# Performance work log

Hardware: AMD Instinct MI355X
Metric: run time of the kernel (lower is better)

## Reference

```python
import jax, jax.numpy as jnp
import numpy as np


def setup_inputs() -> dict:
    key = jax.random.key(0)
    ks = jax.random.split(key, 5)
    B, C_in, C_out, H, W, k = 16, 64, 64, 256, 256, 16
    scale = 1.0 / (C_in * C_out)
    return {
        "u": jax.random.normal(ks[0], (B, C_in, H, W), dtype=jnp.float32),
        "W_pos_re": scale * jax.random.normal(ks[1], (C_in, C_out, k, k), dtype=jnp.float32),
        "W_pos_im": scale * jax.random.normal(ks[2], (C_in, C_out, k, k), dtype=jnp.float32),
        "W_neg_re": scale * jax.random.normal(ks[3], (C_in, C_out, k, k), dtype=jnp.float32),
        "W_neg_im": scale * jax.random.normal(ks[4], (C_in, C_out, k, k), dtype=jnp.float32),
    }


def reference(u, W_pos_re, W_pos_im, W_neg_re, W_neg_im):
    B, C_in, H, W = u.shape
    C_out = W_pos_re.shape[1]
    k = W_pos_re.shape[2]
    W_half = W // 2 + 1
    k_h = min(k, H // 2)
    k_w = min(k, W_half)

    R_pos = (W_pos_re + 1j * W_pos_im)[:, :, :k_h, :k_w]  # (C_in, C_out, k_h, k_w)
    R_neg = (W_neg_re + 1j * W_neg_im)[:, :, :k_h, :k_w]

    u_hat = jnp.fft.rfft2(u, norm="ortho")  # (B, C_in, H, W_half) complex

    # spectral multiply on retained modes only
    top = jnp.einsum("bchw,cohw->bohw", u_hat[:, :, :k_h, :k_w], R_pos)
    bot = jnp.einsum("bchw,cohw->bohw", u_hat[:, :, H - k_h:, :k_w], R_neg)

    v_hat = jnp.zeros((B, C_out, H, W_half), dtype=u_hat.dtype)
    v_hat = v_hat.at[:, :, :k_h, :k_w].set(top)
    v_hat = v_hat.at[:, :, H - k_h:, :k_w].set(bot)

    return jnp.fft.irfft2(v_hat, s=(H, W), norm="ortho")  # (B, C_out, H, W) real
```

## Files before the change

kernel.cpp:

```cpp
#include <hip/hip_runtime.h>


#define B_    16
#define H_    256
#define W_    256

#define OFF_CT 0
#define OFF_ST 256
#define OFF_RP 512
#define RP_SZ  (4096*512*2)
#define OFF_U  (OFF_RP + RP_SZ)
#define U_SZ   (512*1024*2)
#define OFF_V  (OFF_U + U_SZ)

typedef const __attribute__((address_space(1))) void g_void;
typedef __attribute__((address_space(3))) void l_void;

__device__ __forceinline__ void load_lds16(const float* g, float* l) {
    __builtin_amdgcn_global_load_lds((g_void*)g, (l_void*)l, 16, 0, 0);
}

__global__ void k_twiddle(float* __restrict__ ws) {
    int t = threadIdx.x;
    double a = 2.0 * 3.14159265358979323846 * (double)t / 256.0;
    ws[OFF_CT + t] = (float)cos(a);
    ws[OFF_ST + t] = (float)sin(a);
}

__global__ __launch_bounds__(256) void k_repack(const float* __restrict__ wpr,
                                                const float* __restrict__ wpi,
                                                const float* __restrict__ wnr,
                                                const float* __restrict__ wni,
                                                float* __restrict__ ws) {
    int co = blockIdx.x, t = threadIdx.x;
    int wm = t & 15;
    float norm = (wm == 0 ? 1.f : 2.f) * (1.f / 65536.f);
    size_t src = (size_t)co * 256 + t;
    float2* rp = (float2*)(ws + OFF_RP) + (size_t)co * 512;
    rp[t]       = make_float2(wpr[src] * norm, wpi[src] * norm);
    rp[t + 256] = make_float2(wnr[src] * norm, wni[src] * norm);
}

__global__ __launch_bounds__(256) void k_fwd1(const float* __restrict__ u,
                                              const float* __restrict__ ws,
                                              float* __restrict__ P) {
    __shared__ __align__(16) float ut[32][256];
    __shared__ float ct[256], st[256];
    int t = threadIdx.x;
    int bc = blockIdx.x >> 3, ch = blockIdx.x & 7;
    ct[t] = ws[OFF_CT + t];
    st[t] = ws[OFF_ST + t];
    const float* ub = u + (size_t)bc * 65536 + ch * 8192;
    int lane = t & 63, w = t >> 6;
    #pragma unroll
    for (int k = 0; k < 8; ++k) {
        int row = w * 8 + k;
        load_lds16(ub + row * 256 + lane * 4, &ut[row][0]);
    }
    asm volatile("s_waitcnt vmcnt(0)" ::: "memory");
    __syncthreads();

    int yl = t & 31, h = t >> 5;
    int wm0 = 2 * h, wm1 = wm0 + 1;
    int j0 = 2 * yl;
    float t0r = ct[(wm0 * j0) & 255], t0i = -st[(wm0 * j0) & 255];
    float t1r = ct[(wm1 * j0) & 255], t1i = -st[(wm1 * j0) & 255];
    float r0r = ct[wm0], r0i = -st[wm0];
    float r1r = ct[wm1], r1i = -st[wm1];
    float bs  = (h & 1) ? -1.f : 1.f;
    float dsg = (h & 1) ? 1.f : -1.f;
    float p0r = 0.f, p0i = 0.f, p1r = 0.f, p1i = 0.f;
    const float* row = &ut[yl][0];
    #pragma unroll 8
    for (int s = 0; s < 64; ++s) {
        int j = j0 + s;
        float u0 = row[j], u1 = row[j + 64], u2 = row[j + 128];
        float u3 = row[(j + 192) & 255];
        float a = u0 + u2, b = u1 + u3, c = u0 - u2, d = u1 - u3;
        float g0 = fmaf(bs, b, a);
        float g1r = c, g1i = dsg * d;
        p0r = fmaf(g0, t0r, p0r);
        p0i = fmaf(g0, t0i, p0i);
        p1r = fmaf(g1r, t1r, fmaf(-g1i, t1i, p1r));
        p1i = fmaf(g1r, t1i, fmaf( g1i, t1r, p1i));
        float n0r = t0r * r0r - t0i * r0i, n0i = t0r * r0i + t0i * r0r;
        float n1r = t1r * r1r - t1i * r1i, n1i = t1r * r1i + t1i * r1r;
        t0r = n0r; t0i = n0i; t1r = n1r; t1i = n1i;
    }
    int y = ch * 32 + yl;
    ((float4*)P)[((size_t)bc * 256 + y) * 8 + h] = make_float4(p0r, p0i, p1r, p1i);
}

__global__ __launch_bounds__(256) void k_fwd2(const float* __restrict__ P,
                                              float* __restrict__ ws) {
    __shared__ float Pl[256][36];
    __shared__ float ct[256], st[256];
    int t = threadIdx.x, bc = blockIdx.x;
    ct[t] = ws[OFF_CT + t];
    st[t] = ws[OFF_ST + t];
    const float4* Pg = (const float4*)(P + (size_t)bc * 8192);
    #pragma unroll
    for (int k = 0; k < 8; ++k) {
        int f4 = t + 256 * k;
        int y = f4 >> 3, q = f4 & 7;
        *(float4*)&Pl[y][q * 4] = Pg[f4];
    }
    __syncthreads();

    int wm = t & 15;
    int v  = t >> 4;
    int m1 = ((v & 3) << 2) | (v >> 2);
    float r1r = ct[m1], r1i = -st[m1];
    int m2i = (16 - m1) & 255;
    float r2r = ct[m2i], r2i = st[m2i];
    float t1r = 1.f, t1i = 0.f, t2r = 1.f, t2i = 0.f;
    float U1r = 0.f, U1i = 0.f, U2r = 0.f, U2i = 0.f;
    int md = m1 & 3;
    #pragma unroll 4
    for (int yy = 0; yy < 64; ++yy) {
        float2 P0 = *(float2*)&Pl[yy][2 * wm];
        float2 P1 = *(float2*)&Pl[yy + 64][2 * wm];
        float2 P2 = *(float2*)&Pl[yy + 128][2 * wm];
        float2 P3 = *(float2*)&Pl[yy + 192][2 * wm];
        float ar = P0.x + P2.x, ai = P0.y + P2.y;
        float br = P1.x + P3.x, bi = P1.y + P3.y;
        float cr = P0.x - P2.x, ci = P0.y - P2.y;
        float dr = P1.x - P3.x, di = P1.y - P3.y;
        float gr, gi;
        if (md == 0)      { gr = ar + br; gi = ai + bi; }
        else if (md == 1) { gr = cr + di; gi = ci - dr; }
        else if (md == 2) { gr = ar - br; gi = ai - bi; }
        else              { gr = cr - di; gi = ci + dr; }
        U1r = fmaf(gr, t1r, fmaf(-gi, t1i, U1r));
        U1i = fmaf(gr, t1i, fmaf( gi, t1r, U1i));
        U2r = fmaf(gr, t2r, fmaf(-gi, t2i, U2r));
        U2i = fmaf(gr, t2i, fmaf( gi, t2r, U2i));
        float n1r = t1r * r1r - t1i * r1i, n1i = t1r * r1i + t1i * r1r;
        float n2r = t2r * r2r - t2i * r2i, n2i = t2r * r2i + t2i * r2r;
        t1r = n1r; t1i = n1i; t2r = n2r; t2i = n2i;
    }
    float2* U = (float2*)(ws + OFF_U);
    U[(size_t)(m1 * 16 + wm) * 1024 + bc]        = make_float2(U1r, U1i);
    U[(size_t)((m1 + 16) * 16 + wm) * 1024 + bc] = make_float2(U2r, U2i);
}

__global__ __launch_bounds__(256) void k_cgemm(float* __restrict__ ws) {
    __shared__ float2 Ul[1024];
    int mw = blockIdx.x, t = threadIdx.x;
    const float2* Ug = (const float2*)(ws + OFF_U) + (size_t)mw * 1024;
    #pragma unroll
    for (int k = 0; k < 4; ++k) Ul[t + 256 * k] = Ug[t + 256 * k];
    __syncthreads();
    int o = t & 63, bq = t >> 6;
    const float2* rp = (const float2*)(ws + OFF_RP);
    float ar[4] = {0.f, 0.f, 0.f, 0.f}, ai[4] = {0.f, 0.f, 0.f, 0.f};
    #pragma unroll 4
    for (int c = 0; c < 64; ++c) {
        float2 R = rp[(size_t)(c * 64 + o) * 512 + mw];
        #pragma unroll
        for (int j = 0; j < 4; ++j) {
            float2 Uv = Ul[(bq * 4 + j) * 64 + c];
            ar[j] = fmaf(Uv.x, R.x, fmaf(-Uv.y, R.y, ar[j]));
            ai[j] = fmaf(Uv.x, R.y, fmaf( Uv.y, R.x, ai[j]));
        }
    }
    float2* Vg = (float2*)(ws + OFF_V);
    #pragma unroll
    for (int j = 0; j < 4; ++j)
        Vg[(size_t)((bq * 4 + j) * 64 + o) * 512 + mw] = make_float2(ar[j], ai[j]);
}

__global__ __launch_bounds__(256) void k_inv(const float* __restrict__ ws,
                                             float* __restrict__ out) {
    __shared__ float Vl[16][68];
    __shared__ float Tl[4][16][36];
    __shared__ float ct[256], st[256];
    int t = threadIdx.x;
    int bo = blockIdx.x >> 2, q = blockIdx.x & 3;
    ct[t] = ws[OFF_CT + t];
    st[t] = ws[OFF_ST + t];
    {
        const float2* Vg = (const float2*)(ws + OFF_V) + (size_t)bo * 512;
        float2 v0 = Vg[t];
        float2 v1 = Vg[t + 256];
        int m = t >> 4, wmv = t & 15;
        Vl[wmv][2 * m]            = v0.x;  Vl[wmv][2 * m + 1]            = v0.y;
        Vl[wmv][2 * (m + 16)]     = v1.x;  Vl[wmv][2 * (m + 16) + 1]     = v1.y;
    }
    __syncthreads();

    int wm4 = t & 15, yb = t >> 4;
    int y0 = q * 16 + yb;
    float vr[32], vi[32];
    #pragma unroll
    for (int m = 0; m < 32; ++m) { vr[m] = Vl[wm4][2 * m]; vi[m] = Vl[wm4][2 * m + 1]; }
    float cy = ct[y0], sy = st[y0];
    float T0r=0,T0i=0,T1r=0,T1i=0,T2r=0,T2i=0,T3r=0,T3i=0;
    float tr = 1.f, ti = 0.f;
    #pragma unroll
    for (int m = 0; m < 32; ++m) {
        if (m == 16) {
            int i16 = (4096 - 16 * y0) & 255;
            tr = ct[i16]; ti = st[i16];
        }
        float hr = vr[m] * tr - vi[m] * ti;
        float hi = vr[m] * ti + vi[m] * tr;
        const int md = m & 3;
        T0r += hr; T0i += hi;
        if (md == 0)      { T1r += hr; T1i += hi; T2r += hr; T2i += hi; T3r += hr; T3i += hi; }
        else if (md == 1) { T1r -= hi; T1i += hr; T2r -= hr; T2i -= hi; T3r += hi; T3i -= hr; }
        else if (md == 2) { T1r -= hr; T1i -= hi; T2r += hr; T2i += hi; T3r -= hr; T3i -= hi; }
        else              { T1r += hi; T1i -= hr; T2r -= hr; T2i -= hi; T3r -= hi; T3i += hr; }
        float nr = tr * cy - ti * sy, ni = tr * sy + ti * cy;
        tr = nr; ti = ni;
    }
    Tl[0][yb][wm4] = T0r; Tl[0][yb][16 + wm4] = T0i;
    Tl[1][yb][wm4] = T1r; Tl[1][yb][16 + wm4] = T1i;
    Tl[2][yb][wm4] = T2r; Tl[2][yb][16 + wm4] = T2i;
    Tl[3][yb][wm4] = T3r; Tl[3][yb][16 + wm4] = T3i;
    __syncthreads();

    int l = t & 63, wv = t >> 6;
    float c0[16], s0[16];
    #pragma unroll
    for (int wm = 0; wm < 16; ++wm) {
        int idx = (wm * l) & 255;
        c0[wm] = ct[idx]; s0[wm] = st[idx];
    }
    float* ob = out + (size_t)bo * 65536;
    for (int yi = 0; yi < 16; ++yi) {
        int y = wv * 64 + q * 16 + yi;
        float TR[16], TI[16];
        const float4* rowv = (const float4*)&Tl[wv][yi][0];
        #pragma unroll
        for (int qq = 0; qq < 4; ++qq) {
            float4 a = rowv[qq];
            TR[4*qq]=a.x; TR[4*qq+1]=a.y; TR[4*qq+2]=a.z; TR[4*qq+3]=a.w;
            float4 b = rowv[qq + 4];
            TI[4*qq]=b.x; TI[4*qq+1]=b.y; TI[4*qq+2]=b.z; TI[4*qq+3]=b.w;
        }
        #pragma unroll
        for (int k = 0; k < 4; ++k) {
            float a = 0.f;
            #pragma unroll
            for (int wm = 0; wm < 16; ++wm) {
                int p = (k * wm) & 3;
                if (p == 0)      a +=  TR[wm] * c0[wm] - TI[wm] * s0[wm];
                else if (p == 1) a += -TR[wm] * s0[wm] - TI[wm] * c0[wm];
                else if (p == 2) a += -TR[wm] * c0[wm] + TI[wm] * s0[wm];
                else             a +=  TR[wm] * s0[wm] + TI[wm] * c0[wm];
            }
            ob[(size_t)y * 256 + 64 * k + l] = a;
        }
    }
}

extern "C" void kernel_launch(void* const* d_in, const int* in_sizes, int n_in,
                              void* d_out, int out_size, void* d_ws, size_t ws_size,
                              hipStream_t stream) {
    const float* u   = (const float*)d_in[0];
    const float* wpr = (const float*)d_in[1];
    const float* wpi = (const float*)d_in[2];
    const float* wnr = (const float*)d_in[3];
    const float* wni = (const float*)d_in[4];
    float* out = (float*)d_out;
    float* ws  = (float*)d_ws;
    float* P   = (float*)d_out;

    hipLaunchKernelGGL(k_twiddle, dim3(1),    dim3(256), 0, stream, ws);
    hipLaunchKernelGGL(k_repack,  dim3(4096), dim3(256), 0, stream, wpr, wpi, wnr, wni, ws);
    hipLaunchKernelGGL(k_fwd1,    dim3(8192), dim3(256), 0, stream, u, ws, P);
    hipLaunchKernelGGL(k_fwd2,    dim3(1024), dim3(256), 0, stream, P, ws);
    hipLaunchKernelGGL(k_cgemm,   dim3(512),  dim3(256), 0, stream, ws);
    hipLaunchKernelGGL(k_inv,     dim3(4096), dim3(256), 0, stream, ws, out);
}
```

Before: 239.2 us.

## Fuse forward row and column DFT kernels into one per-channel kernel

Merges k_fwd1 and k_fwd2 into a single k_fwd kernel, one block per (batch, channel). The block loops over eight 32-row chunks: it computes the partial row DFT into LDS, then accumulates the column DFT for the retained modes while the next chunk is prefetched asynchronously into LDS. This removes the global round trip of the intermediate P buffer and one kernel launch. In exchange the grid shrinks from 8192 to 1024 blocks, which lowers parallelism, and each block now runs a serial chunk loop with extra barriers.

Result: slower. 254.7 us (+6.5%).

```diff
diff --git a/kernel.cpp b/kernel.cpp
--- a/kernel.cpp
+++ b/kernel.cpp
@@ -41,107 +41,93 @@
     rp[t + 256] = make_float2(wnr[src] * norm, wni[src] * norm);
 }
 
-__global__ __launch_bounds__(256) void k_fwd1(const float* __restrict__ u,
-                                              const float* __restrict__ ws,
-                                              float* __restrict__ P) {
+__global__ __launch_bounds__(256) void k_fwd(const float* __restrict__ u,
+                                             const float* __restrict__ ws,
+                                             float* __restrict__ U) {
     __shared__ __align__(16) float ut[32][256];
-    __shared__ float ct[256], st[256];
-    int t = threadIdx.x;
-    int bc = blockIdx.x >> 3, ch = blockIdx.x & 7;
-    ct[t] = ws[OFF_CT + t];
-    st[t] = ws[OFF_ST + t];
-    const float* ub = u + (size_t)bc * 65536 + ch * 8192;
-    int lane = t & 63, w = t >> 6;
-    #pragma unroll
-    for (int k = 0; k < 8; ++k) {
-        int row = w * 8 + k;
-        load_lds16(ub + row * 256 + lane * 4, &ut[row][0]);
-    }
-    asm volatile("s_waitcnt vmcnt(0)" ::: "memory");
-    __syncthreads();
-
-    int yl = t & 31, h = t >> 5;
-    int wm0 = 2 * h, wm1 = wm0 + 1;
-    int j0 = 2 * yl;
-    float t0r = ct[(wm0 * j0) & 255], t0i = -st[(wm0 * j0) & 255];
-    float t1r = ct[(wm1 * j0) & 255], t1i = -st[(wm1 * j0) & 255];
-    float r0r = ct[wm0], r0i = -st[wm0];
-    float r1r = ct[wm1], r1i = -st[wm1];
-    float bs  = (h & 1) ? -1.f : 1.f;
-    float dsg = (h & 1) ? 1.f : -1.f;
-    float p0r = 0.f, p0i = 0.f, p1r = 0.f, p1i = 0.f;
-    const float* row = &ut[yl][0];
-    #pragma unroll 8
-    for (int s = 0; s < 64; ++s) {
-        int j = j0 + s;
-        float u0 = row[j], u1 = row[j + 64], u2 = row[j + 128];
-        float u3 = row[(j + 192) & 255];
-        float a = u0 + u2, b = u1 + u3, c = u0 - u2, d = u1 - u3;
-        float g0 = fmaf(bs, b, a);
-        float g1r = c, g1i = dsg * d;
-        p0r = fmaf(g0, t0r, p0r);
-        p0i = fmaf(g0, t0i, p0i);
-        p1r = fmaf(g1r, t1r, fmaf(-g1i, t1i, p1r));
-        p1i = fmaf(g1r, t1i, fmaf( g1i, t1r, p1i));
-        float n0r = t0r * r0r - t0i * r0i, n0i = t0r * r0i + t0i * r0r;
-        float n1r = t1r * r1r - t1i * r1i, n1i = t1r * r1i + t1i * r1r;
-        t0r = n0r; t0i = n0i; t1r = n1r; t1i = n1i;
-    }
-    int y = ch * 32 + yl;
-    ((float4*)P)[((size_t)bc * 256 + y) * 8 + h] = make_float4(p0r, p0i, p1r, p1i);
-}
-
-__global__ __launch_bounds__(256) void k_fwd2(const float* __restrict__ P,
-                                              float* __restrict__ ws) {
-    __shared__ float Pl[256][36];
+    __shared__ __align__(16) float Pl[32][36];
     __shared__ float ct[256], st[256];
     int t = threadIdx.x, bc = blockIdx.x;
     ct[t] = ws[OFF_CT + t];
     st[t] = ws[OFF_ST + t];
-    const float4* Pg = (const float4*)(P + (size_t)bc * 8192);
+    const float* ub = u + (size_t)bc * 65536;
+    int lane = t & 63, w = t >> 6;
+
     #pragma unroll
     for (int k = 0; k < 8; ++k) {
-        int f4 = t + 256 * k;
-        int y = f4 >> 3, q = f4 & 7;
-        *(float4*)&Pl[y][q * 4] = Pg[f4];
-    }
-    __syncthreads();
-
-    int wm = t & 15;
-    int v  = t >> 4;
-    int m1 = ((v & 3) << 2) | (v >> 2);
-    float r1r = ct[m1], r1i = -st[m1];
+        int row = w * 8 + k;
+        load_lds16(ub + row * 256 + lane * 4, &ut[row][0]);
+    }
+    __syncthreads();
+
+    int yl = t & 31, h = t >> 5;
+    int wm0 = 2 * h, wm1 = wm0 + 1;
+    int j0 = 2 * yl;
+    float r0r = ct[wm0], r0i = -st[wm0];
+    float r1r = ct[wm1], r1i = -st[wm1];
+    float t0r0 = ct[(wm0 * j0) & 255], t0i0 = -st[(wm0 * j0) & 255];
+    float t1r0 = ct[(wm1 * j0) & 255], t1i0 = -st[(wm1 * j0) & 255];
+    float bs  = (h & 1) ? -1.f : 1.f;
+    float dsg = (h & 1) ? 1.f : -1.f;
+
+    int wm = t & 15, m1 = t >> 4;
+    float q1r = ct[m1], q1i = -st[m1];
     int m2i = (16 - m1) & 255;
-    float r2r = ct[m2i], r2i = st[m2i];
-    float t1r = 1.f, t1i = 0.f, t2r = 1.f, t2i = 0.f;
+    float q2r = ct[m2i], q2i = st[m2i];
+    float w1r = 1.f, w1i = 0.f, w2r = 1.f, w2i = 0.f;
     float U1r = 0.f, U1i = 0.f, U2r = 0.f, U2i = 0.f;
-    int md = m1 & 3;
-    #pragma unroll 4
-    for (int yy = 0; yy < 64; ++yy) {
-        float2 P0 = *(float2*)&Pl[yy][2 * wm];
-        float2 P1 = *(float2*)&Pl[yy + 64][2 * wm];
-        float2 P2 = *(float2*)&Pl[yy + 128][2 * wm];
-        float2 P3 = *(float2*)&Pl[yy + 192][2 * wm];
-        float ar = P0.x + P2.x, ai = P0.y + P2.y;
-        float br = P1.x + P3.x, bi = P1.y + P3.y;
-        float cr = P0.x - P2.x, ci = P0.y - P2.y;
-        float dr = P1.x - P3.x, di = P1.y - P3.y;
-        float gr, gi;
-        if (md == 0)      { gr = ar + br; gi = ai + bi; }
-        else if (md == 1) { gr = cr + di; gi = ci - dr; }
-        else if (md == 2) { gr = ar - br; gi = ai - bi; }
-        else              { gr = cr - di; gi = ci + dr; }
-        U1r = fmaf(gr, t1r, fmaf(-gi, t1i, U1r));
-        U1i = fmaf(gr, t1i, fmaf( gi, t1r, U1i));
-        U2r = fmaf(gr, t2r, fmaf(-gi, t2i, U2r));
-        U2i = fmaf(gr, t2i, fmaf( gi, t2r, U2i));
-        float n1r = t1r * r1r - t1i * r1i, n1i = t1r * r1i + t1i * r1r;
-        float n2r = t2r * r2r - t2i * r2i, n2i = t2r * r2i + t2i * r2r;
-        t1r = n1r; t1i = n1i; t2r = n2r; t2i = n2i;
-    }
-    float2* U = (float2*)(ws + OFF_U);
-    U[(size_t)(m1 * 16 + wm) * 1024 + bc]        = make_float2(U1r, U1i);
-    U[(size_t)((m1 + 16) * 16 + wm) * 1024 + bc] = make_float2(U2r, U2i);
+
+    for (int ch = 0; ch < 8; ++ch) {
+        asm volatile("s_waitcnt vmcnt(0)" ::: "memory");
+        __syncthreads();
+
+        float t0r = t0r0, t0i = t0i0, t1r = t1r0, t1i = t1i0;
+        float p0r = 0.f, p0i = 0.f, p1r = 0.f, p1i = 0.f;
+        const float* row = &ut[yl][0];
+        #pragma unroll 8
+        for (int s = 0; s < 64; ++s) {
+            int j = j0 + s;
+            float u0 = row[j], u1 = row[j + 64], u2 = row[j + 128];
+            float u3 = row[(j + 192) & 255];
+            float a = u0 + u2, b = u1 + u3, c = u0 - u2, d = u1 - u3;
+            float g0 = fmaf(bs, b, a);
+            float g1r = c, g1i = dsg * d;
+            p0r = fmaf(g0, t0r, p0r);
+            p0i = fmaf(g0, t0i, p0i);
+            p1r = fmaf(g1r, t1r, fmaf(-g1i, t1i, p1r));
+            p1i = fmaf(g1r, t1i, fmaf( g1i, t1r, p1i));
+            float n0r = t0r * r0r - t0i * r0i, n0i = t0r * r0i + t0i * r0r;
+            float n1r = t1r * r1r - t1i * r1i, n1i = t1r * r1i + t1i * r1r;
+            t0r = n0r; t0i = n0i; t1r = n1r; t1i = n1i;
+        }
+        *(float4*)&Pl[yl][4 * h] = make_float4(p0r, p0i, p1r, p1i);
+        __syncthreads();
+
+        if (ch < 7) {
+            const float* ub2 = ub + (ch + 1) * 8192;
+            #pragma unroll
+            for (int k = 0; k < 8; ++k) {
+                int rw = w * 8 + k;
+                load_lds16(ub2 + rw * 256 + lane * 4, &ut[rw][0]);
+            }
+        }
+
+        #pragma unroll 4
+        for (int yy = 0; yy < 32; ++yy) {
+            float2 g = *(float2*)&Pl[yy][2 * wm];
+            U1r = fmaf(g.x, w1r, fmaf(-g.y, w1i, U1r));
+            U1i = fmaf(g.x, w1i, fmaf( g.y, w1r, U1i));
+            U2r = fmaf(g.x, w2r, fmaf(-g.y, w2i, U2r));
+            U2i = fmaf(g.x, w2i, fmaf( g.y, w2r, U2i));
+            float n1r = w1r * q1r - w1i * q1i, n1i = w1r * q1i + w1i * q1r;
+            float n2r = w2r * q2r - w2i * q2i, n2i = w2r * q2i + w2i * q2r;
+            w1r = n1r; w1i = n1i; w2r = n2r; w2i = n2i;
+        }
+    }
+
+    float2* Ug = (float2*)U;
+    Ug[(size_t)(m1 * 16 + wm) * 1024 + bc]        = make_float2(U1r, U1i);
+    Ug[(size_t)((m1 + 16) * 16 + wm) * 1024 + bc] = make_float2(U2r, U2i);
 }
 
 __global__ __launch_bounds__(256) void k_cgemm(float* __restrict__ ws) {
@@ -184,8 +170,8 @@
         float2 v0 = Vg[t];
         float2 v1 = Vg[t + 256];
         int m = t >> 4, wmv = t & 15;
-        Vl[wmv][2 * m]            = v0.x;  Vl[wmv][2 * m + 1]            = v0.y;
-        Vl[wmv][2 * (m + 16)]     = v1.x;  Vl[wmv][2 * (m + 16) + 1]     = v1.y;
+        Vl[wmv][2 * m]        = v0.x;  Vl[wmv][2 * m + 1]        = v0.y;
+        Vl[wmv][2 * (m + 16)] = v1.x;  Vl[wmv][2 * (m + 16) + 1] = v1.y;
     }
     __syncthreads();
 
@@ -265,12 +251,10 @@
     const float* wni = (const float*)d_in[4];
     float* out = (float*)d_out;
     float* ws  = (float*)d_ws;
-    float* P   = (float*)d_out;
 
     hipLaunchKernelGGL(k_twiddle, dim3(1),    dim3(256), 0, stream, ws);
     hipLaunchKernelGGL(k_repack,  dim3(4096), dim3(256), 0, stream, wpr, wpi, wnr, wni, ws);
-    hipLaunchKernelGGL(k_fwd1,    dim3(8192), dim3(256), 0, stream, u, ws, P);
-    hipLaunchKernelGGL(k_fwd2,    dim3(1024), dim3(256), 0, stream, P, ws);
+    hipLaunchKernelGGL(k_fwd,     dim3(1024), dim3(256), 0, stream, u, ws, ws + OFF_U);
     hipLaunchKernelGGL(k_cgemm,   dim3(512),  dim3(256), 0, stream, ws);
     hipLaunchKernelGGL(k_inv,     dim3(4096), dim3(256), 0, stream, ws, out);
 }
```

## Remap forward row-DFT threads and vectorize padded LDS reads

Applied to the files above, without the earlier changes.

In the first forward DFT kernel, each group of 8 lanes now shares one input row, with each lane taking its own frequency pair. All lanes walk the row from the start using 128-bit float4 shared-memory loads, instead of staggered scalar loads at per-thread offsets. The shared tile rows are padded to 260 floats so the vector reads from different rows fall in different banks, and the per-thread starting twiddle lookup is removed. This cuts the number of LDS instructions and aims to avoid bank conflicts, at the cost of slightly more shared memory and a different register pattern.

New measurement: 237.6 us. About the same (-0.7%).

```diff
diff --git a/kernel.cpp b/kernel.cpp
--- a/kernel.cpp
+++ b/kernel.cpp
@@ -12,6 +12,8 @@
 #define OFF_U  (OFF_RP + RP_SZ)
 #define U_SZ   (512*1024*2)
 #define OFF_V  (OFF_U + U_SZ)
+
+#define UTP   260
 
 typedef const __attribute__((address_space(1))) void g_void;
 typedef __attribute__((address_space(3))) void l_void;
@@ -44,7 +46,7 @@
 __global__ __launch_bounds__(256) void k_fwd1(const float* __restrict__ u,
                                               const float* __restrict__ ws,
                                               float* __restrict__ P) {
-    __shared__ __align__(16) float ut[32][256];
+    __shared__ __align__(16) float ut[32][UTP];
     __shared__ float ct[256], st[256];
     int t = threadIdx.x;
     int bc = blockIdx.x >> 3, ch = blockIdx.x & 7;
@@ -53,41 +55,50 @@
     const float* ub = u + (size_t)bc * 65536 + ch * 8192;
     int lane = t & 63, w = t >> 6;
     #pragma unroll
-    for (int k = 0; k < 8; ++k) {
-        int row = w * 8 + k;
-        load_lds16(ub + row * 256 + lane * 4, &ut[row][0]);
-    }
+    for (int k = 0; k < 8; ++k)
+        load_lds16(ub + (w * 8 + k) * 256 + lane * 4, &ut[w * 8 + k][0]);
     asm volatile("s_waitcnt vmcnt(0)" ::: "memory");
     __syncthreads();
 
-    int yl = t & 31, h = t >> 5;
+    int h = lane & 7, r8 = lane >> 3;
+    int rowc = w * 8 + r8;
     int wm0 = 2 * h, wm1 = wm0 + 1;
-    int j0 = 2 * yl;
-    float t0r = ct[(wm0 * j0) & 255], t0i = -st[(wm0 * j0) & 255];
-    float t1r = ct[(wm1 * j0) & 255], t1i = -st[(wm1 * j0) & 255];
     float r0r = ct[wm0], r0i = -st[wm0];
     float r1r = ct[wm1], r1i = -st[wm1];
     float bs  = (h & 1) ? -1.f : 1.f;
     float dsg = (h & 1) ? 1.f : -1.f;
+
     float p0r = 0.f, p0i = 0.f, p1r = 0.f, p1i = 0.f;
-    const float* row = &ut[yl][0];
-    #pragma unroll 8
-    for (int s = 0; s < 64; ++s) {
-        int j = j0 + s;
-        float u0 = row[j], u1 = row[j + 64], u2 = row[j + 128];
-        float u3 = row[(j + 192) & 255];
-        float a = u0 + u2, b = u1 + u3, c = u0 - u2, d = u1 - u3;
-        float g0 = fmaf(bs, b, a);
-        float g1r = c, g1i = dsg * d;
-        p0r = fmaf(g0, t0r, p0r);
-        p0i = fmaf(g0, t0i, p0i);
-        p1r = fmaf(g1r, t1r, fmaf(-g1i, t1i, p1r));
-        p1i = fmaf(g1r, t1i, fmaf( g1i, t1r, p1i));
-        float n0r = t0r * r0r - t0i * r0i, n0i = t0r * r0i + t0i * r0r;
-        float n1r = t1r * r1r - t1i * r1i, n1i = t1r * r1i + t1i * r1r;
-        t0r = n0r; t0i = n0i; t1r = n1r; t1i = n1i;
-    }
-    int y = ch * 32 + yl;
+    float t0r = 1.f, t0i = 0.f, t1r = 1.f, t1i = 0.f;
+    const float* rowp = &ut[rowc][0];
+    #pragma unroll 4
+    for (int bat = 0; bat < 16; ++bat) {
+        const float* rp = rowp + 4 * bat;
+        float4 q0 = *(const float4*)(rp);
+        float4 q1 = *(const float4*)(rp + 64);
+        float4 q2 = *(const float4*)(rp + 128);
+        float4 q3 = *(const float4*)(rp + 192);
+        #define PROC_(u0, u1, u2, u3) {                                   \
+            float a_ = (u0) + (u2), b_ = (u1) + (u3);                     \
+            float c_ = (u0) - (u2), d_ = (u1) - (u3);                     \
+            float g0 = fmaf(bs, b_, a_);                                  \
+            float g1r = c_, g1i = dsg * d_;                               \
+            p0r = fmaf(g0, t0r, p0r);                                     \
+            p0i = fmaf(g0, t0i, p0i);                                     \
+            p1r = fmaf(g1r, t1r, fmaf(-g1i, t1i, p1r));                   \
+            p1i = fmaf(g1r, t1i, fmaf( g1i, t1r, p1i));                   \
+            float n0r = t0r * r0r - t0i * r0i;                            \
+            float n0i = t0r * r0i + t0i * r0r;                            \
+            float n1r = t1r * r1r - t1i * r1i;                            \
+            float n1i = t1r * r1i + t1i * r1r;                            \
+            t0r = n0r; t0i = n0i; t1r = n1r; t1i = n1i; }
+        PROC_(q0.x, q1.x, q2.x, q3.x)
+        PROC_(q0.y, q1.y, q2.y, q3.y)
+        PROC_(q0.z, q1.z, q2.z, q3.z)
+        PROC_(q0.w, q1.w, q2.w, q3.w)
+        #undef PROC_
+    }
+    int y = ch * 32 + rowc;
     ((float4*)P)[((size_t)bc * 256 + y) * 8 + h] = make_float4(p0r, p0i, p1r, p1i);
 }
 
@@ -184,8 +195,8 @@
         float2 v0 = Vg[t];
         float2 v1 = Vg[t + 256];
         int m = t >> 4, wmv = t & 15;
-        Vl[wmv][2 * m]            = v0.x;  Vl[wmv][2 * m + 1]            = v0.y;
-        Vl[wmv][2 * (m + 16)]     = v1.x;  Vl[wmv][2 * (m + 16) + 1]     = v1.y;
+        Vl[wmv][2 * m]        = v0.x;  Vl[wmv][2 * m + 1]        = v0.y;
+        Vl[wmv][2 * (m + 16)] = v1.x;  Vl[wmv][2 * (m + 16) + 1] = v1.y;
     }
     __syncthreads();
 
```
